# Performance work log

Measured on AMD Instinct MI355X. Metric: run time of the kernel, lower is better.

## Reference

```python
import jax, jax.numpy as jnp
import numpy as np

ENC = 1024
DEC = 1024


def setup_inputs() -> dict:
    key = jax.random.key(0)
    k = jax.random.split(key, 8)
    s1 = 1.0 / np.sqrt(ENC)
    s2 = 1.0 / np.sqrt(DEC)
    return {
        "encoder_outputs": jax.random.normal(k[0], (32, 2048, ENC), jnp.float32),
        "decoder_output": jax.random.normal(k[1], (32, 1, DEC), jnp.float32),
        "w1": jax.random.uniform(k[2], (ENC, ENC), jnp.float32, -s1, s1),
        "b1": jax.random.uniform(k[3], (ENC,), jnp.float32, -s1, s1),
        "w2": jax.random.uniform(k[4], (DEC, ENC), jnp.float32, -s2, s2),
        "b2": jax.random.uniform(k[5], (ENC,), jnp.float32, -s2, s2),
        "v": jax.random.uniform(k[6], (ENC, 1), jnp.float32, -s1, s1),
        "bv": jax.random.uniform(k[7], (1,), jnp.float32, -s1, s1),
    }


def reference(encoder_outputs, decoder_output, w1, b1, w2, b2, v, bv):
    # [B,1,E] query projection, broadcast-added to [B,S,E] key projection
    w2_dec = jnp.einsum("bqd,de->bqe", decoder_output, w2) + b2
    w1_enc = jnp.einsum("bsd,de->bse", encoder_outputs, w1) + b1
    scores = jnp.einsum("bse,eo->bso", jnp.tanh(w1_enc + w2_dec), v) + bv  # [B,S,1]
    attn = jax.nn.softmax(scores[..., 0], axis=1)  # softmax over sequence dim
    context = jnp.einsum("bs,bse->be", attn, encoder_outputs)  # [B,E]
    return context
```

## Files before the change

### kernel.cpp

```cpp
#include <hip/hip_runtime.h>
#include <hip/hip_bf16.h>


typedef __attribute__((ext_vector_type(8))) short short8;
typedef __attribute__((ext_vector_type(4))) float f32x4;

#define M_TOTAL 65536
#define KDIM    1024

static __device__ inline unsigned int pk2h(float a, float b) {
    unsigned int ua = __builtin_bit_cast(unsigned int, a) + 0x8000u;
    unsigned int ub = __builtin_bit_cast(unsigned int, b) + 0x8000u;
    return __builtin_amdgcn_perm(ub, ua, 0x07060302u);
}

static __device__ inline void async_copy16(const void* g, void* l) {
    __builtin_amdgcn_global_load_lds(
        (const __attribute__((address_space(1))) unsigned int*)g,
        (__attribute__((address_space(3))) unsigned int*)l, 16, 0, 0);
}

__global__ void pack_w1(const float* __restrict__ w1, unsigned short* __restrict__ w1p) {
    __shared__ float tile[32][33];
    const int tx = threadIdx.x, ty = threadIdx.y;
    tile[ty][tx] = w1[(blockIdx.y * 32 + ty) * 1024 + blockIdx.x * 32 + tx];
    __syncthreads();
    const int eo = blockIdx.x * 32 + ty;
    const int dq = blockIdx.y * 32 + tx;
    const unsigned int u = __builtin_bit_cast(unsigned int, tile[tx][ty]) + 0x8000u;
    const unsigned short us = (unsigned short)(u >> 16);
    const int nt = eo >> 7, r = eo & 127;
    const int kc = dq >> 6, c = (dq >> 3) & 7, j = dq & 7;
    const int cs = c ^ (r & 7);
    w1p[(((size_t)(nt * 16 + kc)) << 13) + (r << 6) + (cs << 3) + j] = us;
}

__global__ __launch_bounds__(256) void qq_kern(const float* __restrict__ dec,
                                               const float* __restrict__ w2,
                                               const float* __restrict__ b1,
                                               const float* __restrict__ b2,
                                               float* __restrict__ qq) {
    const int b = blockIdx.y;
    const int e = blockIdx.x * 256 + threadIdx.x;
    const int d0 = blockIdx.z * 256;
    const float* db = dec + b * 1024;
    float acc = (blockIdx.z == 0) ? (b1[e] + b2[e]) : 0.f;
#pragma unroll 8
    for (int d = d0; d < d0 + 256; d++)
        acc = fmaf(db[d], w2[d * 1024 + e], acc);
    atomicAdd(&qq[b * 1024 + e], acc);
}

static __device__ inline void score_epilogue(f32x4 acc[4][4], const float* qqb,
                                             const float* vvec, float* scores,
                                             int m0, int n0, int wm, int wn,
                                             int quad, int lc) {
    const int nb = n0 + wn * 64 + lc;
    float qn[4], vn[4];
#pragma unroll
    for (int ni = 0; ni < 4; ni++) {
        qn[ni] = qqb[nb + ni * 16];
        vn[ni] = vvec[nb + ni * 16];
    }
    float red[16];
#pragma unroll
    for (int mi = 0; mi < 4; mi++) {
#pragma unroll
        for (int r = 0; r < 4; r++) {
            float ssum = 0.f;
#pragma unroll
            for (int ni = 0; ni < 4; ni++) {
                float x = acc[mi][ni][r] + qn[ni];
                float e = __expf(2.0f * x);
                float th = 1.0f - 2.0f / (e + 1.0f);
                ssum = fmaf(th, vn[ni], ssum);
            }
            float t = ssum;
            t += __shfl_xor(t, 1);
            t += __shfl_xor(t, 2);
            t += __shfl_xor(t, 4);
            t += __shfl_xor(t, 8);
            red[mi * 4 + r] = t;
        }
    }
    float myv = red[0];
#pragma unroll
    for (int i = 1; i < 16; i++)
        if (lc == i) myv = red[i];
    atomicAdd(scores + m0 + wm * 64 + (lc >> 2) * 16 + quad * 4 + (lc & 3), myv);
}

__global__ __launch_bounds__(256) void score_gemm(const float* __restrict__ enc,
                                                  const unsigned short* __restrict__ w1p,
                                                  const float* __restrict__ qq,
                                                  const float* __restrict__ vvec,
                                                  float* __restrict__ scores) {
    __shared__ __align__(16) unsigned short As[128 * 64];
    __shared__ __align__(16) unsigned short Bs[128 * 64];

    const int g = blockIdx.x;
    const int mtile = (g & 7) * 64 + (g >> 6);
    const int ntile = (g >> 3) & 7;
    const int m0 = mtile * 128;
    const int b = m0 >> 11;

    const int tid = threadIdx.x;
    const int wid = tid >> 6;
    const int lane = tid & 63;
    const int wm = wid >> 1, wn = wid & 1;
    const int quad = lane >> 4, lc = lane & 15;
    const int swz = lc & 7;
    const int fc0 = ((quad ^ swz) << 3);
    const int fc1 = (((4 + quad) ^ swz) << 3);

    const int sr0 = tid >> 3;
    const int sc = tid & 7;

    f32x4 acc[4][4];
#pragma unroll
    for (int mi = 0; mi < 4; mi++)
#pragma unroll
        for (int ni = 0; ni < 4; ni++)
            acc[mi][ni] = (f32x4){0.f, 0.f, 0.f, 0.f};

    const unsigned short* bbase = w1p + ((size_t)ntile << 17) + (wid << 11) + (lane << 3);
    unsigned short* bdst = &Bs[wid << 11];

    for (int k0 = 0; k0 < KDIM; k0 += 64) {
        __syncthreads();

        const unsigned short* bsrc = bbase + (((size_t)(k0 >> 6)) << 13);
        async_copy16(bsrc, bdst);
        async_copy16(bsrc + 512, bdst + 512);
        async_copy16(bsrc + 1024, bdst + 1024);
        async_copy16(bsrc + 1536, bdst + 1536);

        float4 fv[8];
#pragma unroll
        for (int j = 0; j < 4; j++) {
            const float* src = enc + (size_t)(m0 + sr0 + 32 * j) * 1024 + k0 + sc * 8;
            fv[2 * j]     = *reinterpret_cast<const float4*>(src);
            fv[2 * j + 1] = *reinterpret_cast<const float4*>(src + 4);
        }
#pragma unroll
        for (int j = 0; j < 4; j++) {
            const int r = sr0 + 32 * j;
            uint4 w;
            w.x = pk2h(fv[2 * j].x, fv[2 * j].y);
            w.y = pk2h(fv[2 * j].z, fv[2 * j].w);
            w.z = pk2h(fv[2 * j + 1].x, fv[2 * j + 1].y);
            w.w = pk2h(fv[2 * j + 1].z, fv[2 * j + 1].w);
            *reinterpret_cast<uint4*>(&As[(r << 6) + ((sc ^ (r & 7)) << 3)]) = w;
        }

        __syncthreads();

        short8 af[4], bf[4];
#pragma unroll
        for (int i = 0; i < 4; i++) {
            af[i] = *reinterpret_cast<const short8*>(&As[((wm * 64 + i * 16 + lc) << 6) + fc0]);
            bf[i] = *reinterpret_cast<const short8*>(&Bs[((wn * 64 + i * 16 + lc) << 6) + fc0]);
        }
#pragma unroll
        for (int mi = 0; mi < 4; mi++)
#pragma unroll
            for (int ni = 0; ni < 4; ni++)
                acc[mi][ni] = __builtin_amdgcn_mfma_f32_16x16x32_bf16(af[mi], bf[ni], acc[mi][ni], 0, 0, 0);
#pragma unroll
        for (int i = 0; i < 4; i++) {
            af[i] = *reinterpret_cast<const short8*>(&As[((wm * 64 + i * 16 + lc) << 6) + fc1]);
            bf[i] = *reinterpret_cast<const short8*>(&Bs[((wn * 64 + i * 16 + lc) << 6) + fc1]);
        }
#pragma unroll
        for (int mi = 0; mi < 4; mi++)
#pragma unroll
            for (int ni = 0; ni < 4; ni++)
                acc[mi][ni] = __builtin_amdgcn_mfma_f32_16x16x32_bf16(af[mi], bf[ni], acc[mi][ni], 0, 0, 0);
    }

    score_epilogue(acc, qq + b * 1024, vvec, scores, m0, ntile * 128, wm, wn, quad, lc);
}

__global__ __launch_bounds__(256) void softmax_kern(const float* __restrict__ scores,
                                                    float* __restrict__ attn) {
    const int b = blockIdx.x;
    const int tid = threadIdx.x;
    const int wid = tid >> 6, lane = tid & 63;
    const float* s = scores + b * 2048;
    float x[8];
    float m = -1e30f;
#pragma unroll
    for (int i = 0; i < 8; i++) {
        x[i] = s[tid + i * 256];
        m = fmaxf(m, x[i]);
    }
    for (int off = 1; off < 64; off <<= 1) m = fmaxf(m, __shfl_xor(m, off));
    __shared__ float redm[4];
    if (lane == 0) redm[wid] = m;
    __syncthreads();
    m = fmaxf(fmaxf(redm[0], redm[1]), fmaxf(redm[2], redm[3]));
    float sum = 0.f;
#pragma unroll
    for (int i = 0; i < 8; i++) {
        x[i] = __expf(x[i] - m);
        sum += x[i];
    }
    for (int off = 1; off < 64; off <<= 1) sum += __shfl_xor(sum, off);
    __shared__ float reds[4];
    if (lane == 0) reds[wid] = sum;
    __syncthreads();
    sum = reds[0] + reds[1] + reds[2] + reds[3];
    const float inv = 1.0f / sum;
#pragma unroll
    for (int i = 0; i < 8; i++) attn[b * 2048 + tid + i * 256] = x[i] * inv;
}

__global__ __launch_bounds__(256) void ctx_kern(const float* __restrict__ attn,
                                                const float* __restrict__ enc,
                                                float* __restrict__ out) {
    const int b = blockIdx.y;
    const int sc = blockIdx.x;
    const int tid = threadIdx.x;
    const float* ab = attn + b * 2048 + sc * 64;
    const float* eb = enc + ((size_t)b * 2048 + sc * 64) * 1024 + tid * 4;
    float4 acc = {0.f, 0.f, 0.f, 0.f};
#pragma unroll 16
    for (int s = 0; s < 64; s++) {
        float w = ab[s];
        float4 ev = *reinterpret_cast<const float4*>(eb + (size_t)s * 1024);
        acc.x = fmaf(w, ev.x, acc.x);
        acc.y = fmaf(w, ev.y, acc.y);
        acc.z = fmaf(w, ev.z, acc.z);
        acc.w = fmaf(w, ev.w, acc.w);
    }
    float* op = out + b * 1024 + tid * 4;
    atomicAdd(op + 0, acc.x);
    atomicAdd(op + 1, acc.y);
    atomicAdd(op + 2, acc.z);
    atomicAdd(op + 3, acc.w);
}

extern "C" void kernel_launch(void* const* d_in, const int* in_sizes, int n_in,
                              void* d_out, int out_size, void* d_ws, size_t ws_size,
                              hipStream_t stream) {
    const float* enc = (const float*)d_in[0];
    const float* dec = (const float*)d_in[1];
    const float* w1  = (const float*)d_in[2];
    const float* b1  = (const float*)d_in[3];
    const float* w2  = (const float*)d_in[4];
    const float* b2  = (const float*)d_in[5];
    const float* v   = (const float*)d_in[6];
    float* out = (float*)d_out;

    char* ws = (char*)d_ws;
    unsigned short* w1p = (unsigned short*)ws;
    float* qq     = (float*)(ws + (2u << 20));
    float* scores = (float*)(ws + (2u << 20) + (128u << 10));
    float* attn   = scores + M_TOTAL;

    hipMemsetAsync(qq, 0, (128u << 10) + M_TOTAL * sizeof(float), stream);
    hipMemsetAsync(out, 0, 32 * 1024 * sizeof(float), stream);

    pack_w1<<<dim3(32, 32), dim3(32, 32), 0, stream>>>(w1, w1p);
    qq_kern<<<dim3(4, 32, 4), 256, 0, stream>>>(dec, w2, b1, b2, qq);
    score_gemm<<<4096, 256, 0, stream>>>(enc, w1p, qq, v, scores);
    softmax_kern<<<32, 256, 0, stream>>>(scores, attn);
    ctx_kern<<<dim3(32, 32), 256, 0, stream>>>(attn, enc, out);
}
```

Baseline: 655.5 us.

## Stage full 64-row encoder tile in LDS once, stream W1 fragments from global

The score GEMM is restructured so each 512-thread block converts a 64x1024 slab of encoder rows to bf16 in LDS one time and covers all 1024 output columns. Each wave reads its W1 fragments directly from global memory in a new fragment-ready packed layout, double-buffered in registers, and MFMA issue priority is raised with s_setprio. The previous design reread the encoder tile once per N-tile (8x) and synchronized every K step. This removes that re-reading and the per-iteration barriers. In exchange the block uses a large LDS allocation (128KB) and more accumulator registers, and W1 reads now come from L2 rather than LDS.

```diff
diff --git a/kernel.cpp b/kernel.cpp
--- a/kernel.cpp
+++ b/kernel.cpp
@@ -14,25 +14,20 @@
     return __builtin_amdgcn_perm(ub, ua, 0x07060302u);
 }
 
-static __device__ inline void async_copy16(const void* g, void* l) {
-    __builtin_amdgcn_global_load_lds(
-        (const __attribute__((address_space(1))) unsigned int*)g,
-        (__attribute__((address_space(3))) unsigned int*)l, 16, 0, 0);
-}
-
-__global__ void pack_w1(const float* __restrict__ w1, unsigned short* __restrict__ w1p) {
-    __shared__ float tile[32][33];
-    const int tx = threadIdx.x, ty = threadIdx.y;
-    tile[ty][tx] = w1[(blockIdx.y * 32 + ty) * 1024 + blockIdx.x * 32 + tx];
-    __syncthreads();
-    const int eo = blockIdx.x * 32 + ty;
-    const int dq = blockIdx.y * 32 + tx;
-    const unsigned int u = __builtin_bit_cast(unsigned int, tile[tx][ty]) + 0x8000u;
-    const unsigned short us = (unsigned short)(u >> 16);
-    const int nt = eo >> 7, r = eo & 127;
-    const int kc = dq >> 6, c = (dq >> 3) & 7, j = dq & 7;
-    const int cs = c ^ (r & 7);
-    w1p[(((size_t)(nt * 16 + kc)) << 13) + (r << 6) + (cs << 3) + j] = us;
+__global__ __launch_bounds__(64) void pack_w1(const float* __restrict__ w1,
+                                              unsigned short* __restrict__ w1p) {
+    const int nt = blockIdx.x;
+    const int kt = blockIdx.y;
+    const int l  = threadIdx.x;
+    const int n  = nt * 16 + (l & 15);
+    const int kb = kt * 32 + (l >> 4) * 8;
+    const float* s = w1 + (size_t)kb * 1024 + n;
+    uint4 wv;
+    wv.x = pk2h(s[0],    s[1024]);
+    wv.y = pk2h(s[2048], s[3072]);
+    wv.z = pk2h(s[4096], s[5120]);
+    wv.w = pk2h(s[6144], s[7168]);
+    *reinterpret_cast<uint4*>(w1p + (((size_t)(kt * 64 + nt)) << 9) + (l << 3)) = wv;
 }
 
 __global__ __launch_bounds__(256) void qq_kern(const float* __restrict__ dec,
@@ -51,16 +46,105 @@
     atomicAdd(&qq[b * 1024 + e], acc);
 }
 
-static __device__ inline void score_epilogue(f32x4 acc[4][4], const float* qqb,
-                                             const float* vvec, float* scores,
-                                             int m0, int n0, int wm, int wn,
-                                             int quad, int lc) {
-    const int nb = n0 + wn * 64 + lc;
-    float qn[4], vn[4];
-#pragma unroll
-    for (int ni = 0; ni < 4; ni++) {
-        qn[ni] = qqb[nb + ni * 16];
-        vn[ni] = vvec[nb + ni * 16];
+__global__ __launch_bounds__(512, 2) void score_gemm(const float* __restrict__ enc,
+                                                     const unsigned short* __restrict__ w1p,
+                                                     const float* __restrict__ qq,
+                                                     const float* __restrict__ vvec,
+                                                     float* __restrict__ scores) {
+    __shared__ __align__(16) unsigned short As[64 * 1024];
+
+    const int m0 = blockIdx.x << 6;
+    const int b = m0 >> 11;
+    const int tid = threadIdx.x;
+    const int wid = tid >> 6;
+    const int lane = tid & 63;
+    const int quad = lane >> 4, lc = lane & 15;
+
+    {
+        const int r  = tid >> 3;
+        const int c8 = tid & 7;
+        const int sw = c8 ^ (r & 7);
+        const float* src0 = enc + (size_t)(m0 + r) * 1024 + (c8 << 3);
+        unsigned short* dst0 = As + (r << 10) + (sw << 3);
+#pragma unroll 4
+        for (int w = 0; w < 16; w++) {
+            const float* s = src0 + (w << 6);
+            float4 f0 = *reinterpret_cast<const float4*>(s);
+            float4 f1 = *reinterpret_cast<const float4*>(s + 4);
+            uint4 pv;
+            pv.x = pk2h(f0.x, f0.y);
+            pv.y = pk2h(f0.z, f0.w);
+            pv.z = pk2h(f1.x, f1.y);
+            pv.w = pk2h(f1.z, f1.w);
+            *reinterpret_cast<uint4*>(dst0 + (w << 6)) = pv;
+        }
+    }
+
+    f32x4 acc[4][8];
+#pragma unroll
+    for (int mi = 0; mi < 4; mi++)
+#pragma unroll
+        for (int ni = 0; ni < 8; ni++)
+            acc[mi][ni] = (f32x4){0.f, 0.f, 0.f, 0.f};
+
+    __syncthreads();
+
+    const unsigned short* bb = w1p + ((size_t)wid << 12) + (lane << 3);
+
+    short8 bA[8], bB[8];
+#pragma unroll
+    for (int ni = 0; ni < 8; ni++)
+        bA[ni] = *reinterpret_cast<const short8*>(bb + ni * 512);
+
+    for (int kt = 0; kt < 32; kt += 2) {
+#pragma unroll
+        for (int ni = 0; ni < 8; ni++)
+            bB[ni] = *reinterpret_cast<const short8*>(bb + (kt + 1) * 32768 + ni * 512);
+
+        short8 af[4];
+        {
+            const int c = kt * 4 + quad;
+            const int off = ((c & ~7) | ((c ^ lc) & 7)) << 3;
+#pragma unroll
+            for (int mi = 0; mi < 4; mi++)
+                af[mi] = *reinterpret_cast<const short8*>(&As[((mi * 16 + lc) << 10) + off]);
+        }
+        __builtin_amdgcn_s_setprio(1);
+#pragma unroll
+        for (int mi = 0; mi < 4; mi++)
+#pragma unroll
+            for (int ni = 0; ni < 8; ni++)
+                acc[mi][ni] = __builtin_amdgcn_mfma_f32_16x16x32_bf16(af[mi], bA[ni], acc[mi][ni], 0, 0, 0);
+        __builtin_amdgcn_s_setprio(0);
+
+        if (kt < 30) {
+#pragma unroll
+            for (int ni = 0; ni < 8; ni++)
+                bA[ni] = *reinterpret_cast<const short8*>(bb + (kt + 2) * 32768 + ni * 512);
+        }
+        {
+            const int c = kt * 4 + 4 + quad;
+            const int off = ((c & ~7) | ((c ^ lc) & 7)) << 3;
+#pragma unroll
+            for (int mi = 0; mi < 4; mi++)
+                af[mi] = *reinterpret_cast<const short8*>(&As[((mi * 16 + lc) << 10) + off]);
+        }
+        __builtin_amdgcn_s_setprio(1);
+#pragma unroll
+        for (int mi = 0; mi < 4; mi++)
+#pragma unroll
+            for (int ni = 0; ni < 8; ni++)
+                acc[mi][ni] = __builtin_amdgcn_mfma_f32_16x16x32_bf16(af[mi], bB[ni], acc[mi][ni], 0, 0, 0);
+        __builtin_amdgcn_s_setprio(0);
+    }
+
+    const float* qb = qq + (b << 10) + (wid << 7) + lc;
+    const float* vb = vvec + (wid << 7) + lc;
+    float qn[8], vn[8];
+#pragma unroll
+    for (int ni = 0; ni < 8; ni++) {
+        qn[ni] = qb[ni << 4];
+        vn[ni] = vb[ni << 4];
     }
     float red[16];
 #pragma unroll
@@ -69,7 +153,7 @@
         for (int r = 0; r < 4; r++) {
             float ssum = 0.f;
 #pragma unroll
-            for (int ni = 0; ni < 4; ni++) {
+            for (int ni = 0; ni < 8; ni++) {
                 float x = acc[mi][ni][r] + qn[ni];
                 float e = __expf(2.0f * x);
                 float th = 1.0f - 2.0f / (e + 1.0f);
@@ -87,98 +171,7 @@
 #pragma unroll
     for (int i = 1; i < 16; i++)
         if (lc == i) myv = red[i];
-    atomicAdd(scores + m0 + wm * 64 + (lc >> 2) * 16 + quad * 4 + (lc & 3), myv);
-}
-
-__global__ __launch_bounds__(256) void score_gemm(const float* __restrict__ enc,
-                                                  const unsigned short* __restrict__ w1p,
-                                                  const float* __restrict__ qq,
-                                                  const float* __restrict__ vvec,
-                                                  float* __restrict__ scores) {
-    __shared__ __align__(16) unsigned short As[128 * 64];
-    __shared__ __align__(16) unsigned short Bs[128 * 64];
-
-    const int g = blockIdx.x;
-    const int mtile = (g & 7) * 64 + (g >> 6);
-    const int ntile = (g >> 3) & 7;
-    const int m0 = mtile * 128;
-    const int b = m0 >> 11;
-
-    const int tid = threadIdx.x;
-    const int wid = tid >> 6;
-    const int lane = tid & 63;
-    const int wm = wid >> 1, wn = wid & 1;
-    const int quad = lane >> 4, lc = lane & 15;
-    const int swz = lc & 7;
-    const int fc0 = ((quad ^ swz) << 3);
-    const int fc1 = (((4 + quad) ^ swz) << 3);
-
-    const int sr0 = tid >> 3;
-    const int sc = tid & 7;
-
-    f32x4 acc[4][4];
-#pragma unroll
-    for (int mi = 0; mi < 4; mi++)
-#pragma unroll
-        for (int ni = 0; ni < 4; ni++)
-            acc[mi][ni] = (f32x4){0.f, 0.f, 0.f, 0.f};
-
-    const unsigned short* bbase = w1p + ((size_t)ntile << 17) + (wid << 11) + (lane << 3);
-    unsigned short* bdst = &Bs[wid << 11];
-
-    for (int k0 = 0; k0 < KDIM; k0 += 64) {
-        __syncthreads();
-
-        const unsigned short* bsrc = bbase + (((size_t)(k0 >> 6)) << 13);
-        async_copy16(bsrc, bdst);
-        async_copy16(bsrc + 512, bdst + 512);
-        async_copy16(bsrc + 1024, bdst + 1024);
-        async_copy16(bsrc + 1536, bdst + 1536);
-
-        float4 fv[8];
-#pragma unroll
-        for (int j = 0; j < 4; j++) {
-            const float* src = enc + (size_t)(m0 + sr0 + 32 * j) * 1024 + k0 + sc * 8;
-            fv[2 * j]     = *reinterpret_cast<const float4*>(src);
-            fv[2 * j + 1] = *reinterpret_cast<const float4*>(src + 4);
-        }
-#pragma unroll
-        for (int j = 0; j < 4; j++) {
-            const int r = sr0 + 32 * j;
-            uint4 w;
-            w.x = pk2h(fv[2 * j].x, fv[2 * j].y);
-            w.y = pk2h(fv[2 * j].z, fv[2 * j].w);
-            w.z = pk2h(fv[2 * j + 1].x, fv[2 * j + 1].y);
-            w.w = pk2h(fv[2 * j + 1].z, fv[2 * j + 1].w);
-            *reinterpret_cast<uint4*>(&As[(r << 6) + ((sc ^ (r & 7)) << 3)]) = w;
-        }
-
-        __syncthreads();
-
-        short8 af[4], bf[4];
-#pragma unroll
-        for (int i = 0; i < 4; i++) {
-            af[i] = *reinterpret_cast<const short8*>(&As[((wm * 64 + i * 16 + lc) << 6) + fc0]);
-            bf[i] = *reinterpret_cast<const short8*>(&Bs[((wn * 64 + i * 16 + lc) << 6) + fc0]);
-        }
-#pragma unroll
-        for (int mi = 0; mi < 4; mi++)
-#pragma unroll
-            for (int ni = 0; ni < 4; ni++)
-                acc[mi][ni] = __builtin_amdgcn_mfma_f32_16x16x32_bf16(af[mi], bf[ni], acc[mi][ni], 0, 0, 0);
-#pragma unroll
-        for (int i = 0; i < 4; i++) {
-            af[i] = *reinterpret_cast<const short8*>(&As[((wm * 64 + i * 16 + lc) << 6) + fc1]);
-            bf[i] = *reinterpret_cast<const short8*>(&Bs[((wn * 64 + i * 16 + lc) << 6) + fc1]);
-        }
-#pragma unroll
-        for (int mi = 0; mi < 4; mi++)
-#pragma unroll
-            for (int ni = 0; ni < 4; ni++)
-                acc[mi][ni] = __builtin_amdgcn_mfma_f32_16x16x32_bf16(af[mi], bf[ni], acc[mi][ni], 0, 0, 0);
-    }
-
-    score_epilogue(acc, qq + b * 1024, vvec, scores, m0, ntile * 128, wm, wn, quad, lc);
+    atomicAdd(scores + m0 + (lc >> 2) * 16 + quad * 4 + (lc & 3), myv);
 }
 
 __global__ __launch_bounds__(256) void softmax_kern(const float* __restrict__ scores,
@@ -261,9 +254,9 @@
     hipMemsetAsync(qq, 0, (128u << 10) + M_TOTAL * sizeof(float), stream);
     hipMemsetAsync(out, 0, 32 * 1024 * sizeof(float), stream);
 
-    pack_w1<<<dim3(32, 32), dim3(32, 32), 0, stream>>>(w1, w1p);
+    pack_w1<<<dim3(64, 32), 64, 0, stream>>>(w1, w1p);
     qq_kern<<<dim3(4, 32, 4), 256, 0, stream>>>(dec, w2, b1, b2, qq);
-    score_gemm<<<4096, 256, 0, stream>>>(enc, w1p, qq, v, scores);
+    score_gemm<<<1024, 512, 0, stream>>>(enc, w1p, qq, v, scores);
     softmax_kern<<<32, 256, 0, stream>>>(scores, attn);
     ctx_kern<<<dim3(32, 32), 256, 0, stream>>>(attn, enc, out);
 }
```

Result: faster. 566.2 us (-13.6%).
